# Performance work log

Hardware: AMD Instinct MI355X
Metric: run time of the kernel (lower is better)

The kernel has to match this reference:

```python
import jax, jax.numpy as jnp
import numpy as np

N_P = 100000   # number of platforms (rows of pF)
N_M = 100000   # number of modules (rows of M)
R = 64         # embedding rank r = M.shape[1]
S = 3          # number of interference terms s
B = 500000     # batch of (i, j, k) index triples
ALPHA = 0.001
BETA = 0.001


def setup_inputs() -> dict:
    key = jax.random.key(0)
    k1, k2, k3 = jax.random.split(key, 3)
    pF = jax.random.normal(k1, (N_P, R * (1 + 2 * S)), dtype=jnp.float32)
    M = jax.random.normal(k2, (N_M, R), dtype=jnp.float32)
    ijk = jax.random.randint(k3, (B, 3), 0, N_M)  # i,j,k indices; k==-1 would mask
    return {"pF": pF, "M": M, "ijk": ijk}


def reference(pF, M, ijk):
    # MatrixFactorizationIF.__call__ with baseline=None, full=False, log=True.
    r = M.shape[1]
    i, j, k = ijk[:, 0], ijk[:, 1], ijk[:, 2]
    pFi = pF[i]                                        # [B, r*(1+2s)] gather
    Pi = pFi[:, :r]                                    # [B, r]
    Vs = BETA * pFi[:, r:(1 + S) * r].reshape(-1, r, S)  # [B, r, s]
    Vg = BETA * pFi[:, (1 + S) * r:].reshape(-1, r, S)   # [B, r, s]
    Mj = M[j]                                          # [B, r]
    kc = jnp.where(k < 0, 0, k)                        # clamp invalid k for gather
    Mk = M[kc]                                         # [B, r]
    mask = (k != -1).astype(M.dtype)                   # 1[valid k]
    a = jnp.einsum('brs,br->bs', Vs, Mj)               # V_s[i]^T m_j
    g = jnp.einsum('brs,br->bs', Vg, Mk)               # V_g[i]^T m_k
    mFm = mask * jnp.sum(a * g, axis=-1)               # interference term
    return ALPHA * jnp.sum(Pi * Mj, axis=-1) + mFm     # C_bar = 0 (no baseline)
```

## Files before the change

kernel.cpp:

```cpp
#include <hip/hip_runtime.h>

constexpr float ALPHA = 0.001f;
constexpr float BETA  = 0.001f;
constexpr int R   = 64;
constexpr int S   = 3;
constexpr int PFW = R * (1 + 2 * S);
constexpr int BSH  = 7;
constexpr int MAXB = 800;
constexpr int SBLK = 256;

__device__ __forceinline__ float bfhi(unsigned u) {
    union { unsigned u; float f; } c; c.u = u & 0xffff0000u; return c.f;
}
__device__ __forceinline__ float bflo(unsigned u) {
    union { unsigned u; float f; } c; c.u = u << 16; return c.f;
}

__global__ __launch_bounds__(256) void convM_kernel(const float* __restrict__ M,
                                                    uint4* __restrict__ Mb, int n8) {
    int idx = blockIdx.x * 256 + threadIdx.x;
    if (idx >= n8) return;
    const float* src = M + (size_t)idx * 8;
    unsigned w[8];
    #pragma unroll
    for (int t = 0; t < 8; ++t) {
        union { float f; unsigned u; } c;
        c.f = __builtin_nontemporal_load(src + t);
        w[t] = (c.u + 0x7fffu + ((c.u >> 16) & 1u)) >> 16;
    }
    Mb[idx] = make_uint4(w[0] | (w[1] << 16), w[2] | (w[3] << 16),
                         w[4] | (w[5] << 16), w[6] | (w[7] << 16));
}

__global__ __launch_bounds__(256) void hist_kernel(const int* __restrict__ ijk, int B,
                                                   int chunk, int nb, int* __restrict__ hist) {
    __shared__ int lh[MAXB];
    for (int t = threadIdx.x; t < nb; t += blockDim.x) lh[t] = 0;
    __syncthreads();
    const int lo = blockIdx.x * chunk, hi = min(B, lo + chunk);
    for (int idx = lo + threadIdx.x; idx < hi; idx += blockDim.x)
        atomicAdd(&lh[ijk[3 * idx] >> BSH], 1);
    __syncthreads();
    for (int t = threadIdx.x; t < nb; t += blockDim.x)
        if (lh[t]) atomicAdd(&hist[t], lh[t]);
}

__global__ __launch_bounds__(1024) void scan_kernel(const int* __restrict__ hist,
                                                    int* __restrict__ cursor, int nb) {
    __shared__ int buf[1024];
    int t = threadIdx.x;
    int own = (t < nb) ? hist[t] : 0;
    buf[t] = own;
    __syncthreads();
    for (int d = 1; d < 1024; d <<= 1) {
        int v = (t >= d) ? buf[t - d] : 0;
        __syncthreads();
        buf[t] += v;
        __syncthreads();
    }
    if (t < nb) cursor[t] = buf[t] - own;
}

__global__ __launch_bounds__(256) void scatter_kernel(const int* __restrict__ ijk, int B,
                                                      int chunk, int nb,
                                                      int* __restrict__ cursor,
                                                      int4* __restrict__ sorted) {
    __shared__ int cnt[MAXB];
    __shared__ int base[MAXB];
    __shared__ int rnk[MAXB];
    for (int t = threadIdx.x; t < nb; t += blockDim.x) { cnt[t] = 0; rnk[t] = 0; }
    __syncthreads();
    const int lo = blockIdx.x * chunk, hi = min(B, lo + chunk);
    for (int idx = lo + threadIdx.x; idx < hi; idx += blockDim.x)
        atomicAdd(&cnt[ijk[3 * idx] >> BSH], 1);
    __syncthreads();
    for (int t = threadIdx.x; t < nb; t += blockDim.x)
        if (cnt[t]) base[t] = atomicAdd(&cursor[t], cnt[t]);
    __syncthreads();
    for (int idx = lo + threadIdx.x; idx < hi; idx += blockDim.x) {
        const int i = ijk[3 * idx], j = ijk[3 * idx + 1], k = ijk[3 * idx + 2];
        const int bkt = i >> BSH;
        const int p = base[bkt] + atomicAdd(&rnk[bkt], 1);
        sorted[p] = make_int4(i, j, k, idx);
    }
}

__global__ __launch_bounds__(256) void mf_if_kernel(
    const float* __restrict__ pF,
    const float* __restrict__ M,
    const uint2* __restrict__ Mb,
    const int4*  __restrict__ sorted,
    const int*   __restrict__ ijk,
    float* __restrict__ out,
    int B, int nwg)
{
    const int orig = blockIdx.x;
    const int q = nwg >> 3, r = nwg & 7;
    const int xcd = orig & 7;
    const int wgid = (xcd < r ? xcd * (q + 1) : r * (q + 1) + (xcd - r) * q) + (orig >> 3);

    const int sub = threadIdx.x & 15;
    const long pos = (long)wgid * 16 + (threadIdx.x >> 4);
    if (pos >= B) return;

    int4 s;
    if (sorted) {
        const unsigned long long* sp =
            reinterpret_cast<const unsigned long long*>(sorted + pos);
        unsigned long long lo = __builtin_nontemporal_load(sp);
        unsigned long long hi = __builtin_nontemporal_load(sp + 1);
        s.x = (int)lo; s.y = (int)(lo >> 32); s.z = (int)hi; s.w = (int)(hi >> 32);
    } else {
        s = make_int4(ijk[3 * pos], ijk[3 * pos + 1], ijk[3 * pos + 2], (int)pos);
    }

    const int kc = (s.z < 0) ? 0 : s.z;

    const float4* pFi = reinterpret_cast<const float4*>(pF + (size_t)s.x * PFW);

    float4 mj, mk;
    if (Mb) {
        const uint2 uj = Mb[(size_t)s.y * 16 + sub];
        const uint2 uk = Mb[(size_t)kc  * 16 + sub];
        mj = make_float4(bflo(uj.x), bfhi(uj.x), bflo(uj.y), bfhi(uj.y));
        mk = make_float4(bflo(uk.x), bfhi(uk.x), bflo(uk.y), bfhi(uk.y));
    } else {
        mj = reinterpret_cast<const float4*>(M + (size_t)s.y * R)[sub];
        mk = reinterpret_cast<const float4*>(M + (size_t)kc  * R)[sub];
    }

    const float4 pi = pFi[sub];
    float p = pi.x * mj.x + pi.y * mj.y + pi.z * mj.z + pi.w * mj.w;

    const float4 v0 = pFi[16 + 3 * sub + 0];
    const float4 v1 = pFi[16 + 3 * sub + 1];
    const float4 v2 = pFi[16 + 3 * sub + 2];
    float a0 = v0.x * mj.x + v0.w * mj.y + v1.z * mj.z + v2.y * mj.w;
    float a1 = v0.y * mj.x + v1.x * mj.y + v1.w * mj.z + v2.z * mj.w;
    float a2 = v0.z * mj.x + v1.y * mj.y + v2.x * mj.z + v2.w * mj.w;

    const float4 w0 = pFi[64 + 3 * sub + 0];
    const float4 w1 = pFi[64 + 3 * sub + 1];
    const float4 w2 = pFi[64 + 3 * sub + 2];
    float g0 = w0.x * mk.x + w0.w * mk.y + w1.z * mk.z + w2.y * mk.w;
    float g1 = w0.y * mk.x + w1.x * mk.y + w1.w * mk.z + w2.z * mk.w;
    float g2 = w0.z * mk.x + w1.y * mk.y + w2.x * mk.z + w2.w * mk.w;

    #pragma unroll
    for (int off = 8; off >= 1; off >>= 1) {
        p  += __shfl_xor(p,  off);
        a0 += __shfl_xor(a0, off);
        a1 += __shfl_xor(a1, off);
        a2 += __shfl_xor(a2, off);
        g0 += __shfl_xor(g0, off);
        g1 += __shfl_xor(g1, off);
        g2 += __shfl_xor(g2, off);
    }

    if (sub == 0) {
        const float mfm = (s.z != -1)
            ? (BETA * BETA) * (a0 * g0 + a1 * g1 + a2 * g2) : 0.0f;
        out[s.w] = ALPHA * p + mfm;
    }
}

extern "C" void kernel_launch(void* const* d_in, const int* in_sizes, int n_in,
                              void* d_out, int out_size, void* d_ws, size_t ws_size,
                              hipStream_t stream) {
    const float* pF  = (const float*)d_in[0];
    const float* M   = (const float*)d_in[1];
    const int*   ijk = (const int*)d_in[2];
    float* out = (float*)d_out;

    const int B   = in_sizes[2] / 3;
    const int N_P = in_sizes[0] / PFW;
    const int N_M = in_sizes[1] / R;
    const int nb  = (N_P + (1 << BSH) - 1) >> BSH;

    const size_t sorted_off = 16 * 1024;
    const size_t mb_off     = sorted_off + (size_t)B * sizeof(int4);
    const size_t need_sort  = mb_off;
    const size_t need_full  = mb_off + (size_t)N_M * R * 2;

    int4*  sorted = nullptr;
    uint2* Mb     = nullptr;

    if (nb <= MAXB && ws_size >= need_sort) {
        int* hist   = (int*)d_ws;
        int* cursor = hist + 1024;
        sorted = (int4*)((char*)d_ws + sorted_off);
        const int chunk = (B + SBLK - 1) / SBLK;

        hipMemsetAsync(hist, 0, 1024 * sizeof(int), stream);
        hist_kernel<<<SBLK, 256, 0, stream>>>(ijk, B, chunk, nb, hist);
        scan_kernel<<<1, 1024, 0, stream>>>(hist, cursor, nb);
        scatter_kernel<<<SBLK, 256, 0, stream>>>(ijk, B, chunk, nb, cursor, sorted);
    }
    if (ws_size >= need_full) {
        Mb = (uint2*)((char*)d_ws + mb_off);
        const int n8 = N_M * R / 8;
        convM_kernel<<<(n8 + 255) / 256, 256, 0, stream>>>(M, (uint4*)Mb, n8);
    }

    const int nwg = (B + 15) / 16;
    mf_if_kernel<<<nwg, 256, 0, stream>>>(pF, M, Mb, sorted, ijk, out, B, nwg);
}
```

Baseline: 99.33 us.

## Fuse M conversion into scatter kernel and use 8 lanes per sample

Merges the bf16 conversion of M into the scatter launch as extra blocks, which removes one kernel launch and lets the two phases run concurrently. The main kernel now handles each sample with 8 lanes instead of 16, using wider 16-byte loads of Mb and more work per thread. Its reduction shrinks by combining a and g products before the final shuffle. The sorted-index load switches from nontemporal loads to a plain int4 load. The older fp32 path is kept as a fallback when workspace is insufficient.

```diff
diff --git a/kernel.cpp b/kernel.cpp
--- a/kernel.cpp
+++ b/kernel.cpp
@@ -16,22 +16,6 @@
     union { unsigned u; float f; } c; c.u = u << 16; return c.f;
 }
 
-__global__ __launch_bounds__(256) void convM_kernel(const float* __restrict__ M,
-                                                    uint4* __restrict__ Mb, int n8) {
-    int idx = blockIdx.x * 256 + threadIdx.x;
-    if (idx >= n8) return;
-    const float* src = M + (size_t)idx * 8;
-    unsigned w[8];
-    #pragma unroll
-    for (int t = 0; t < 8; ++t) {
-        union { float f; unsigned u; } c;
-        c.f = __builtin_nontemporal_load(src + t);
-        w[t] = (c.u + 0x7fffu + ((c.u >> 16) & 1u)) >> 16;
-    }
-    Mb[idx] = make_uint4(w[0] | (w[1] << 16), w[2] | (w[3] << 16),
-                         w[4] | (w[5] << 16), w[6] | (w[7] << 16));
-}
-
 __global__ __launch_bounds__(256) void hist_kernel(const int* __restrict__ ijk, int B,
                                                    int chunk, int nb, int* __restrict__ hist) {
     __shared__ int lh[MAXB];
@@ -61,10 +45,27 @@
     if (t < nb) cursor[t] = buf[t] - own;
 }
 
-__global__ __launch_bounds__(256) void scatter_kernel(const int* __restrict__ ijk, int B,
-                                                      int chunk, int nb,
-                                                      int* __restrict__ cursor,
-                                                      int4* __restrict__ sorted) {
+__global__ __launch_bounds__(256) void scatconv_kernel(
+    const int* __restrict__ ijk, int B, int chunk, int nb,
+    int* __restrict__ cursor, int4* __restrict__ sorted,
+    const float* __restrict__ M, uint4* __restrict__ Mb, int n8)
+{
+    if (blockIdx.x >= SBLK) {
+        const int idx = (blockIdx.x - SBLK) * 256 + threadIdx.x;
+        if (idx < n8) {
+            const float* src = M + (size_t)idx * 8;
+            unsigned w[8];
+            #pragma unroll
+            for (int t = 0; t < 8; ++t) {
+                union { float f; unsigned u; } c;
+                c.f = __builtin_nontemporal_load(src + t);
+                w[t] = (c.u + 0x7fffu + ((c.u >> 16) & 1u)) >> 16;
+            }
+            Mb[idx] = make_uint4(w[0] | (w[1] << 16), w[2] | (w[3] << 16),
+                                 w[4] | (w[5] << 16), w[6] | (w[7] << 16));
+        }
+        return;
+    }
     __shared__ int cnt[MAXB];
     __shared__ int base[MAXB];
     __shared__ int rnk[MAXB];
@@ -85,12 +86,10 @@
     }
 }
 
-__global__ __launch_bounds__(256) void mf_if_kernel(
+__global__ __launch_bounds__(256) void mf8_kernel(
     const float* __restrict__ pF,
-    const float* __restrict__ M,
-    const uint2* __restrict__ Mb,
+    const uint4* __restrict__ Mb,
     const int4*  __restrict__ sorted,
-    const int*   __restrict__ ijk,
     float* __restrict__ out,
     int B, int nwg)
 {
@@ -99,68 +98,103 @@
     const int xcd = orig & 7;
     const int wgid = (xcd < r ? xcd * (q + 1) : r * (q + 1) + (xcd - r) * q) + (orig >> 3);
 
-    const int sub = threadIdx.x & 15;
-    const long pos = (long)wgid * 16 + (threadIdx.x >> 4);
+    const int sub = threadIdx.x & 7;
+    const long pos = (long)wgid * 32 + (threadIdx.x >> 3);
     if (pos >= B) return;
 
-    int4 s;
-    if (sorted) {
-        const unsigned long long* sp =
-            reinterpret_cast<const unsigned long long*>(sorted + pos);
-        unsigned long long lo = __builtin_nontemporal_load(sp);
-        unsigned long long hi = __builtin_nontemporal_load(sp + 1);
-        s.x = (int)lo; s.y = (int)(lo >> 32); s.z = (int)hi; s.w = (int)(hi >> 32);
-    } else {
-        s = make_int4(ijk[3 * pos], ijk[3 * pos + 1], ijk[3 * pos + 2], (int)pos);
-    }
-
+    const int4 s = sorted[pos];
     const int kc = (s.z < 0) ? 0 : s.z;
 
     const float4* pFi = reinterpret_cast<const float4*>(pF + (size_t)s.x * PFW);
 
-    float4 mj, mk;
-    if (Mb) {
-        const uint2 uj = Mb[(size_t)s.y * 16 + sub];
-        const uint2 uk = Mb[(size_t)kc  * 16 + sub];
-        mj = make_float4(bflo(uj.x), bfhi(uj.x), bflo(uj.y), bfhi(uj.y));
-        mk = make_float4(bflo(uk.x), bfhi(uk.x), bflo(uk.y), bfhi(uk.y));
-    } else {
-        mj = reinterpret_cast<const float4*>(M + (size_t)s.y * R)[sub];
-        mk = reinterpret_cast<const float4*>(M + (size_t)kc  * R)[sub];
-    }
-
-    const float4 pi = pFi[sub];
-    float p = pi.x * mj.x + pi.y * mj.y + pi.z * mj.z + pi.w * mj.w;
-
-    const float4 v0 = pFi[16 + 3 * sub + 0];
-    const float4 v1 = pFi[16 + 3 * sub + 1];
-    const float4 v2 = pFi[16 + 3 * sub + 2];
-    float a0 = v0.x * mj.x + v0.w * mj.y + v1.z * mj.z + v2.y * mj.w;
-    float a1 = v0.y * mj.x + v1.x * mj.y + v1.w * mj.z + v2.z * mj.w;
-    float a2 = v0.z * mj.x + v1.y * mj.y + v2.x * mj.z + v2.w * mj.w;
-
-    const float4 w0 = pFi[64 + 3 * sub + 0];
-    const float4 w1 = pFi[64 + 3 * sub + 1];
-    const float4 w2 = pFi[64 + 3 * sub + 2];
-    float g0 = w0.x * mk.x + w0.w * mk.y + w1.z * mk.z + w2.y * mk.w;
-    float g1 = w0.y * mk.x + w1.x * mk.y + w1.w * mk.z + w2.z * mk.w;
-    float g2 = w0.z * mk.x + w1.y * mk.y + w2.x * mk.z + w2.w * mk.w;
+    const uint4 uj = Mb[(size_t)s.y * 8 + sub];
+    const uint4 uk = Mb[(size_t)kc  * 8 + sub];
+    const float4 pi0 = pFi[2 * sub], pi1 = pFi[2 * sub + 1];
+    const float4 v0 = pFi[16 + 6 * sub + 0], v1 = pFi[16 + 6 * sub + 1];
+    const float4 v2 = pFi[16 + 6 * sub + 2], v3 = pFi[16 + 6 * sub + 3];
+    const float4 v4 = pFi[16 + 6 * sub + 4], v5 = pFi[16 + 6 * sub + 5];
+    const float4 w0 = pFi[64 + 6 * sub + 0], w1 = pFi[64 + 6 * sub + 1];
+    const float4 w2 = pFi[64 + 6 * sub + 2], w3 = pFi[64 + 6 * sub + 3];
+    const float4 w4 = pFi[64 + 6 * sub + 4], w5 = pFi[64 + 6 * sub + 5];
+
+    const float mj0 = bflo(uj.x), mj1 = bfhi(uj.x), mj2 = bflo(uj.y), mj3 = bfhi(uj.y);
+    const float mj4 = bflo(uj.z), mj5 = bfhi(uj.z), mj6 = bflo(uj.w), mj7 = bfhi(uj.w);
+    const float mk0 = bflo(uk.x), mk1 = bfhi(uk.x), mk2 = bflo(uk.y), mk3 = bfhi(uk.y);
+    const float mk4 = bflo(uk.z), mk5 = bfhi(uk.z), mk6 = bflo(uk.w), mk7 = bfhi(uk.w);
+
+    float p = pi0.x * mj0 + pi0.y * mj1 + pi0.z * mj2 + pi0.w * mj3
+            + pi1.x * mj4 + pi1.y * mj5 + pi1.z * mj6 + pi1.w * mj7;
+
+    float a0 = v0.x * mj0 + v0.w * mj1 + v1.z * mj2 + v2.y * mj3
+             + v3.x * mj4 + v3.w * mj5 + v4.z * mj6 + v5.y * mj7;
+    float a1 = v0.y * mj0 + v1.x * mj1 + v1.w * mj2 + v2.z * mj3
+             + v3.y * mj4 + v4.x * mj5 + v4.w * mj6 + v5.z * mj7;
+    float a2 = v0.z * mj0 + v1.y * mj1 + v2.x * mj2 + v2.w * mj3
+             + v3.z * mj4 + v4.y * mj5 + v5.x * mj6 + v5.w * mj7;
+
+    float g0 = w0.x * mk0 + w0.w * mk1 + w1.z * mk2 + w2.y * mk3
+             + w3.x * mk4 + w3.w * mk5 + w4.z * mk6 + w5.y * mk7;
+    float g1 = w0.y * mk0 + w1.x * mk1 + w1.w * mk2 + w2.z * mk3
+             + w3.y * mk4 + w4.x * mk5 + w4.w * mk6 + w5.z * mk7;
+    float g2 = w0.z * mk0 + w1.y * mk1 + w2.x * mk2 + w2.w * mk3
+             + w3.z * mk4 + w4.y * mk5 + w5.x * mk6 + w5.w * mk7;
 
     #pragma unroll
-    for (int off = 8; off >= 1; off >>= 1) {
+    for (int off = 4; off >= 1; off >>= 1) {
         p  += __shfl_xor(p,  off);
         a0 += __shfl_xor(a0, off);
         a1 += __shfl_xor(a1, off);
         a2 += __shfl_xor(a2, off);
-        g0 += __shfl_xor(g0, off);
-        g1 += __shfl_xor(g1, off);
-        g2 += __shfl_xor(g2, off);
-    }
+    }
+    float h = a0 * g0 + a1 * g1 + a2 * g2;
+    #pragma unroll
+    for (int off = 4; off >= 1; off >>= 1)
+        h += __shfl_xor(h, off);
 
     if (sub == 0) {
-        const float mfm = (s.z != -1)
-            ? (BETA * BETA) * (a0 * g0 + a1 * g1 + a2 * g2) : 0.0f;
+        const float mfm = (s.z != -1) ? (BETA * BETA) * h : 0.0f;
         out[s.w] = ALPHA * p + mfm;
+    }
+}
+
+__global__ __launch_bounds__(256) void mf_if_kernel(
+    const float* __restrict__ pF,
+    const float* __restrict__ M,
+    const int*   __restrict__ ijk,
+    float* __restrict__ out,
+    int B)
+{
+    const int sub = threadIdx.x & 15;
+    const long pos = (long)blockIdx.x * 16 + (threadIdx.x >> 4);
+    if (pos >= B) return;
+
+    const int i = ijk[3 * pos], j = ijk[3 * pos + 1], k = ijk[3 * pos + 2];
+    const int kc = (k < 0) ? 0 : k;
+
+    const float4* pFi = reinterpret_cast<const float4*>(pF + (size_t)i * PFW);
+    const float4 mj = reinterpret_cast<const float4*>(M + (size_t)j  * R)[sub];
+    const float4 mk = reinterpret_cast<const float4*>(M + (size_t)kc * R)[sub];
+
+    const float4 pi = pFi[sub];
+    float p = pi.x * mj.x + pi.y * mj.y + pi.z * mj.z + pi.w * mj.w;
+    const float4 v0 = pFi[16 + 3 * sub], v1 = pFi[17 + 3 * sub], v2 = pFi[18 + 3 * sub];
+    float a0 = v0.x * mj.x + v0.w * mj.y + v1.z * mj.z + v2.y * mj.w;
+    float a1 = v0.y * mj.x + v1.x * mj.y + v1.w * mj.z + v2.z * mj.w;
+    float a2 = v0.z * mj.x + v1.y * mj.y + v2.x * mj.z + v2.w * mj.w;
+    const float4 w0 = pFi[64 + 3 * sub], w1 = pFi[65 + 3 * sub], w2 = pFi[66 + 3 * sub];
+    float g0 = w0.x * mk.x + w0.w * mk.y + w1.z * mk.z + w2.y * mk.w;
+    float g1 = w0.y * mk.x + w1.x * mk.y + w1.w * mk.z + w2.z * mk.w;
+    float g2 = w0.z * mk.x + w1.y * mk.y + w2.x * mk.z + w2.w * mk.w;
+
+    #pragma unroll
+    for (int off = 8; off >= 1; off >>= 1) {
+        p  += __shfl_xor(p,  off);
+        a0 += __shfl_xor(a0, off); a1 += __shfl_xor(a1, off); a2 += __shfl_xor(a2, off);
+        g0 += __shfl_xor(g0, off); g1 += __shfl_xor(g1, off); g2 += __shfl_xor(g2, off);
+    }
+    if (sub == 0) {
+        const float mfm = (k != -1) ? (BETA * BETA) * (a0 * g0 + a1 * g1 + a2 * g2) : 0.0f;
+        out[pos] = ALPHA * p + mfm;
     }
 }
 
@@ -179,29 +213,26 @@
 
     const size_t sorted_off = 16 * 1024;
     const size_t mb_off     = sorted_off + (size_t)B * sizeof(int4);
-    const size_t need_sort  = mb_off;
     const size_t need_full  = mb_off + (size_t)N_M * R * 2;
 
-    int4*  sorted = nullptr;
-    uint2* Mb     = nullptr;
-
-    if (nb <= MAXB && ws_size >= need_sort) {
-        int* hist   = (int*)d_ws;
-        int* cursor = hist + 1024;
-        sorted = (int4*)((char*)d_ws + sorted_off);
+    if (nb <= MAXB && ws_size >= need_full) {
+        int*   hist   = (int*)d_ws;
+        int*   cursor = (int*)((char*)d_ws + 4096);
+        int4*  sorted = (int4*)((char*)d_ws + sorted_off);
+        uint4* Mb     = (uint4*)((char*)d_ws + mb_off);
         const int chunk = (B + SBLK - 1) / SBLK;
-
-        hipMemsetAsync(hist, 0, 1024 * sizeof(int), stream);
+        const int n8 = N_M * R / 8;
+        const int convBlocks = (n8 + 255) / 256;
+
+        hipMemsetAsync(d_ws, 0, 8192, stream);
         hist_kernel<<<SBLK, 256, 0, stream>>>(ijk, B, chunk, nb, hist);
         scan_kernel<<<1, 1024, 0, stream>>>(hist, cursor, nb);
-        scatter_kernel<<<SBLK, 256, 0, stream>>>(ijk, B, chunk, nb, cursor, sorted);
-    }
-    if (ws_size >= need_full) {
-        Mb = (uint2*)((char*)d_ws + mb_off);
-        const int n8 = N_M * R / 8;
-        convM_kernel<<<(n8 + 255) / 256, 256, 0, stream>>>(M, (uint4*)Mb, n8);
-    }
-
-    const int nwg = (B + 15) / 16;
-    mf_if_kernel<<<nwg, 256, 0, stream>>>(pF, M, Mb, sorted, ijk, out, B, nwg);
-}
+        scatconv_kernel<<<SBLK + convBlocks, 256, 0, stream>>>(
+            ijk, B, chunk, nb, cursor, sorted, M, Mb, n8);
+
+        const int nwg = (B + 31) / 32;
+        mf8_kernel<<<nwg, 256, 0, stream>>>(pF, Mb, sorted, out, B, nwg);
+    } else {
+        mf_if_kernel<<<(B + 15) / 16, 256, 0, stream>>>(pF, M, ijk, out, B);
+    }
+}
```

Result: slower. 137.6 us (+38.5%).
